# Kernel optimization log

Measured on AMD Instinct MI355X. Metric: run time of the kernel, lower is better.

The kernel has to match this reference:

```python
import jax, jax.numpy as jnp
import numpy as np

HW = 65536      # height*width = 256*256
C = 200         # spectral channels
NSP = 1024      # superpixels
E = 524288      # pixel-graph edges
D = 128         # hidden dim (hard-coded in module)
NCLS = 16
BN_EPS = 1e-5
LRELU = 0.01    # LeakyReLU default slope


def _l2norm(x):
    # F.normalize(x, dim=1)
    n = jnp.linalg.norm(x, axis=1, keepdims=True)
    return x / jnp.maximum(n, 1e-12)


def _bn(x):
    # BatchNorm1d, training-mode batch stats, default affine (gamma=1, beta=0)
    m = x.mean(0)
    v = x.var(0)
    return (x - m) * jax.lax.rsqrt(v + BN_EPS)


def _leaky(x):
    return jnp.where(x >= 0, x, LRELU * x)


def _gcn_conv(x, src, dst, W, b, n):
    # PyG GCNConv: add self-loops, sym-normalized aggregation, then bias
    xw = x @ W                                   # [n, D]
    deg = jnp.zeros((n,), x.dtype).at[dst].add(1.0) + 1.0  # incl. self-loop
    dinv = jax.lax.rsqrt(deg)
    norm = dinv[src] * dinv[dst]                 # [E]
    agg = jax.ops.segment_sum(xw[src] * norm[:, None], dst, num_segments=n)
    return agg + xw / deg[:, None] + b           # self-loop norm = 1/deg


def setup_inputs() -> dict:
    key = jax.random.key(0)
    ks = jax.random.split(key, 16)
    x = jax.random.normal(ks[0], (HW, C), jnp.float32)
    # one-hot superpixel assignment (every superpixel non-empty)
    seg = jnp.arange(HW, dtype=jnp.int32) % NSP
    seg = jax.random.permutation(ks[1], seg)
    Q = jax.nn.one_hot(seg, NSP, dtype=jnp.float32)
    # sparse-ish symmetric superpixel adjacency, normalized as in GCNLayer.__init__
    B = (jax.random.uniform(ks[2], (NSP, NSP)) < 0.01).astype(jnp.float32)
    A = jnp.maximum(B, B.T) * (1.0 - jnp.eye(NSP, dtype=jnp.float32))
    Ah = A + jnp.eye(NSP, dtype=jnp.float32)
    dinv = jax.lax.rsqrt(Ah.sum(1))
    A_norm = dinv[:, None] * Ah * dinv[None, :]
    edge_index = jax.random.randint(ks[3], (2, E), 0, HW, dtype=jnp.int32)
    s = 0.05
    return {
        'x': x, 'Q': Q, 'A_norm': A_norm, 'edge_index': edge_index,
        'prelin_W': jax.random.normal(ks[4], (C, D), jnp.float32) * s,
        'prelin_b': jnp.zeros((D,), jnp.float32),
        'gcn1_W': jax.random.normal(ks[5], (D, D), jnp.float32) * s,
        'gcn1_b': jnp.zeros((D,), jnp.float32),
        'gcn2_W': jax.random.normal(ks[6], (D, D), jnp.float32) * s,
        'gcn2_b': jnp.zeros((D,), jnp.float32),
        'mpnn1_W': jax.random.normal(ks[7], (D, D), jnp.float32) * s,
        'mpnn1_b': jnp.zeros((D,), jnp.float32),
        'mpnn2_W': jax.random.normal(ks[8], (D, D), jnp.float32) * s,
        'mpnn2_b': jnp.zeros((D,), jnp.float32),
        'out_W': jax.random.normal(ks[9], (D, NCLS), jnp.float32) * s,
        'out_b': jnp.zeros((NCLS,), jnp.float32),
    }


def reference(x, Q, A_norm, edge_index, prelin_W, prelin_b,
              gcn1_W, gcn1_b, gcn2_W, gcn2_b,
              mpnn1_W, mpnn1_b, mpnn2_W, mpnn2_b, out_W, out_b):
    # prelin + BN on pixels
    h = _bn(x @ prelin_W + prelin_b)             # [HW, D]
    # superpixel pooling (column-normalized Q), dense matmul as in original
    norm_col_Q = Q / Q.sum(0, keepdims=True)     # [HW, NSP]
    sp = norm_col_Q.T @ h                        # [NSP, D]

    def gcn_layer(H, W, b):
        return _leaky(A_norm @ (_bn(_l2norm(H)) @ W + b))

    H1 = gcn_layer(gcn_layer(sp, gcn1_W, gcn1_b), gcn2_W, gcn2_b)
    gcn_result = Q @ H1                          # unpool to pixels [HW, D]

    src, dst = edge_index[0], edge_index[1]

    def mpnn_layer(H, W, b):
        return _leaky(_gcn_conv(_bn(_l2norm(H)), src, dst, W, b, HW))

    m = mpnn_layer(mpnn_layer(h, mpnn1_W, mpnn1_b), mpnn2_W, mpnn2_b)
    logits = (m + gcn_result) @ out_W + out_b    # [HW, NCLS]
    return jax.nn.softmax(logits, axis=-1)
```

## Files before the change

### kernel.cpp

```cpp
#include <hip/hip_runtime.h>

#define HW 65536
#define NSP 1024
#define NE 524288
#define NCLS 16
#define BN_EPS 1e-5f
#define LSLOPE 0.01f

typedef unsigned short u16;
typedef short s16x8 __attribute__((ext_vector_type(8)));
typedef u16 u16x8 __attribute__((ext_vector_type(8)));
typedef u16 u16x4 __attribute__((ext_vector_type(4)));
typedef float f32x4 __attribute__((ext_vector_type(4)));

__device__ inline u16 f2b(float x) {
  unsigned int u = __float_as_uint(x);
  unsigned int r = ((u >> 16) & 1u) + 0x7FFFu;
  return (u16)((u + r) >> 16);
}
__device__ inline float b2f(u16 u) { return __uint_as_float(((unsigned int)u) << 16); }

struct P {
  const float *x, *Q, *A_norm;
  const int *e_src, *e_dst;
  const float *preW, *preB;
  const float *g1W, *g1b, *g2W, *g2b;
  const float *m1W, *m1b, *m2W, *m2b;
  const float *oW, *ob;
  float *outp;
  float *bufA, *bufB;
  int *cntd, *cntinv;
  float *stats;
  float *spDp, *spHp;
  int *seg, *seginv, *offp, *cur;
  float *dinv;
  int2 *e2;
  int *bsum;
  float *spA, *spC, *spDa;
  float *WppG1, *WppG2;
  u16 *WTm1, *WTm2, *WTpre;
  float *cvG1, *bpG1, *cvG2, *bpG2, *cvM1, *bpM1, *cvM2, *bpM2;
  float *invG1, *invG2, *invM1;
  u16 *xb, *xwB, *bufN;
};

#define S_A(p)  ((p).stats + 0*256)
#define S_G1(p) ((p).stats + 1*256)
#define S_G2(p) ((p).stats + 2*256)
#define S_M1(p) ((p).stats + 3*256)
#define S_M2(p) ((p).stats + 4*256)

#define NQB 4096
#define NDB (NE / 256)
#define CXB (HW * 56 / 256)
#define CWB 112

__global__ __launch_bounds__(256) void k_setup(P p) {
  int b = blockIdx.x, t = threadIdx.x;
  if (b < NQB) {
    const float4* Q4 = (const float4*)p.Q;
    const int n4 = HW * NSP / 4;
    for (int i = b * 256 + t; i < n4; i += NQB * 256) {
      float4 q = Q4[i];
      int base = i * 4;
      #pragma unroll
      for (int e = 0; e < 4; ++e) {
        float qv = (e == 0) ? q.x : (e == 1) ? q.y : (e == 2) ? q.z : q.w;
        if (qv > 0.5f) {
          int idx = base + e;
          int r = idx >> 10, s = idx & (NSP - 1);
          p.seg[r] = s;
          int pos = atomicAdd(&p.cntinv[s], 1);
          p.seginv[s * 64 + pos] = r;
        }
      }
    }
  } else if (b < NQB + NDB) {
    int e = (b - NQB) * 256 + t;
    if (e < NE) atomicAdd(&p.cntd[p.e_dst[e]], 1);
  } else if (b < NQB + NDB + CXB) {
    int g = (b - NQB - NDB) * 256 + t;
    int row = g / 56, qd = g - row * 56;
    int k0 = qd * 4;
    u16x4 o;
    if (k0 < 200) {
      float4 v = *(const float4*)&p.x[(size_t)row * 200 + k0];
      o[0] = f2b(v.x); o[1] = f2b(v.y); o[2] = f2b(v.z); o[3] = f2b(v.w);
    } else { o[0] = 0; o[1] = 0; o[2] = 0; o[3] = 0; }
    *(u16x4*)&p.xb[(size_t)row * 224 + k0] = o;
  } else {
    int g = (b - NQB - NDB - CXB) * 256 + t;
    if (g < 128 * 224) {
      int n = g / 224, k = g - n * 224;
      p.WTpre[g] = (k < 200) ? f2b(p.preW[(size_t)k * 128 + n]) : (u16)0;
    }
  }
}

__device__ void dev_scan_a(P& p, int b, char* smem) {
  int* s = (int*)smem;
  int t = threadIdx.x;
  int i = b * 256 + t;
  int v = p.cntd[i];
  s[t] = v; __syncthreads();
  for (int o = 1; o < 256; o <<= 1) {
    int x = (t >= o) ? s[t - o] : 0;
    __syncthreads();
    s[t] += x;
    __syncthreads();
  }
  p.offp[i] = s[t] - v;
  if (t == 255) p.bsum[b] = s[t];
}

__device__ void dev_scan_c2(P& p, int b, char* smem) {
  int* w4 = (int*)smem;
  int t = threadIdx.x;
  int v = (t < b) ? p.bsum[t] : 0;
  #pragma unroll
  for (int o = 1; o < 64; o <<= 1) v += __shfl_xor(v, o);
  if ((t & 63) == 0) w4[t >> 6] = v;
  __syncthreads();
  int base = w4[0] + w4[1] + w4[2] + w4[3];
  int i = b * 256 + t;
  int ov = p.offp[i] + base;
  p.offp[i] = ov;
  p.cur[i] = ov;
  p.dinv[i] = rsqrtf((float)p.cntd[i] + 1.0f);
  if (i == 0) p.offp[HW] = NE;
}

__device__ void dev_scatter(P& p, int b) {
  int e = b * 256 + threadIdx.x;
  if (e < NE) {
    int d = p.e_dst[e], s = p.e_src[e];
    float w = p.dinv[d] * p.dinv[s];
    int pos = atomicAdd(&p.cur[d], 1);
    p.e2[pos] = make_int2(s, __float_as_int(w));
  }
}

__device__ void dev_mgemm(const void* Ap, int a_bf16, int lda,
                          const u16* WT, int ldb, int K,
                          const float* bias, const float* cvec, const float* invn,
                          void* Cp, int c_bf16,
                          float* sums, float* sumsq, int bid, char* smem) {
  u16* As = (u16*)smem;
  u16* Bs = (u16*)(smem + 10240);
  float* lsum = (float*)(smem + 30720);
  float* lssq = lsum + 128;
  int t = threadIdx.x;
  if (sums && t < 128) { lsum[t] = 0.f; lssq[t] = 0.f; }
  int row0 = bid * 64;
  int ar = t >> 2, ak = (t & 3) * 8;
  u16x8 aReg; u16x8 bReg[2];

  auto loadRegs = [&](int k0) {
    if (a_bf16) {
      aReg = *(const u16x8*)((const u16*)Ap + (size_t)(row0 + ar) * lda + k0 + ak);
    } else {
      const float* ap = (const float*)Ap + (size_t)(row0 + ar) * lda + k0 + ak;
      float4 f0 = *(const float4*)ap;
      float4 f1 = *(const float4*)(ap + 4);
      u16x8 v;
      v[0] = f2b(f0.x); v[1] = f2b(f0.y); v[2] = f2b(f0.z); v[3] = f2b(f0.w);
      v[4] = f2b(f1.x); v[5] = f2b(f1.y); v[6] = f2b(f1.z); v[7] = f2b(f1.w);
      aReg = v;
    }
    #pragma unroll
    for (int it = 0; it < 2; ++it) {
      int slot = t + it * 256;
      int bn = slot >> 2, kg = (slot & 3) * 8;
      bReg[it] = *(const u16x8*)(WT + (size_t)bn * ldb + k0 + kg);
    }
  };
  auto dsWrite = [&](int bq) {
    *(u16x8*)&As[(bq * 64 + ar) * 40 + ak] = aReg;
    #pragma unroll
    for (int it = 0; it < 2; ++it) {
      int slot = t + it * 256;
      int bn = slot >> 2, kg = (slot & 3) * 8;
      *(u16x8*)&Bs[(bq * 128 + bn) * 40 + kg] = bReg[it];
    }
  };

  int lane = t & 63, wv = t >> 6;
  int m0 = (wv >> 1) * 32, n0 = (wv & 1) * 64;
  int fr = lane & 15, fk = (lane >> 4) * 8;
  f32x4 acc[2][4];
  #pragma unroll
  for (int mt = 0; mt < 2; ++mt)
    #pragma unroll
    for (int nt = 0; nt < 4; ++nt)
      acc[mt][nt] = (f32x4){0.f, 0.f, 0.f, 0.f};

  int nch = K >> 5;
  loadRegs(0);
  int cur = 0;
  for (int ch = 0; ch < nch; ++ch) {
    dsWrite(cur);
    __syncthreads();
    if (ch + 1 < nch) loadRegs((ch + 1) << 5);
    s16x8 afr0 = *(const s16x8*)&As[(cur * 64 + m0 + fr) * 40 + fk];
    s16x8 afr1 = *(const s16x8*)&As[(cur * 64 + m0 + 16 + fr) * 40 + fk];
    s16x8 bfr[4];
    #pragma unroll
    for (int nt = 0; nt < 4; ++nt)
      bfr[nt] = *(const s16x8*)&Bs[(cur * 128 + n0 + nt * 16 + fr) * 40 + fk];
    #pragma unroll
    for (int nt = 0; nt < 4; ++nt) {
      acc[0][nt] = __builtin_amdgcn_mfma_f32_16x16x32_bf16(afr0, bfr[nt], acc[0][nt], 0, 0, 0);
      acc[1][nt] = __builtin_amdgcn_mfma_f32_16x16x32_bf16(afr1, bfr[nt], acc[1][nt], 0, 0, 0);
    }
    cur ^= 1;
  }

  float bb4[4], cv4[4];
  #pragma unroll
  for (int nt = 0; nt < 4; ++nt) {
    int c = n0 + nt * 16 + fr;
    bb4[nt] = bias ? bias[c] : 0.f;
    cv4[nt] = cvec ? cvec[c] : 0.f;
  }
  int rg = lane >> 4;
  float cs4[4] = {}, cq4[4] = {};
  #pragma unroll
  for (int mt = 0; mt < 2; ++mt) {
    int rbase = row0 + m0 + mt * 16 + rg * 4;
    float inr[4];
    #pragma unroll
    for (int j = 0; j < 4; ++j) inr[j] = invn ? invn[rbase + j] : 1.f;
    #pragma unroll
    for (int nt = 0; nt < 4; ++nt) {
      int c = n0 + nt * 16 + fr;
      #pragma unroll
      for (int j = 0; j < 4; ++j) {
        float xv = inr[j] * (acc[mt][nt][j] - cv4[nt]) + bb4[nt];
        if (sums) { cs4[nt] += xv; cq4[nt] += xv * xv; }
        if (c_bf16) ((u16*)Cp)[(size_t)(rbase + j) * 128 + c] = f2b(xv);
        else        ((float*)Cp)[(size_t)(rbase + j) * 128 + c] = xv;
      }
    }
  }
  if (sums) {
    __syncthreads();
    #pragma unroll
    for (int nt = 0; nt < 4; ++nt) {
      int c = n0 + nt * 16 + fr;
      atomicAdd(&lsum[c], cs4[nt]);
      atomicAdd(&lssq[c], cq4[nt]);
    }
    __syncthreads();
    if (t < 128) { atomicAdd(&sums[t], lsum[t]); atomicAdd(&sumsq[t], lssq[t]); }
  }
}

__device__ void dev_pool2(P& p, int sp, char* smem) {
  float4* part = (float4*)smem;
  int t = threadIdx.x;
  int l32 = t & 31, g = t >> 5;
  int cnt = p.cntinv[sp];
  const float4* y4 = (const float4*)p.bufA;
  const int* lst = p.seginv + sp * 64;
  float4 acc = make_float4(0.f, 0.f, 0.f, 0.f);
  int r = g;
  for (; r + 8 < cnt; r += 16) {
    int i0 = lst[r], i1 = lst[r + 8];
    float4 a = y4[(size_t)i0 * 32 + l32];
    float4 b = y4[(size_t)i1 * 32 + l32];
    acc.x += a.x + b.x; acc.y += a.y + b.y;
    acc.z += a.z + b.z; acc.w += a.w + b.w;
  }
  for (; r < cnt; r += 8) {
    float4 a = y4[(size_t)lst[r] * 32 + l32];
    acc.x += a.x; acc.y += a.y; acc.z += a.z; acc.w += a.w;
  }
  part[g * 32 + l32] = acc;
  __syncthreads();
  if (g == 0) {
    float4 s = part[l32];
    #pragma unroll
    for (int q = 1; q < 8; ++q) {
      float4 pp = part[q * 32 + l32];
      s.x += pp.x; s.y += pp.y; s.z += pp.z; s.w += pp.w;
    }
    int d0 = l32 * 4;
    const float* sAs = S_A(p);
    const float* sAq = S_A(p) + 128;
    float4 ss = *(const float4*)&sAs[d0];
    float4 sq = *(const float4*)&sAq[d0];
    float inv = 1.0f / (float)cnt;
    float4 o;
    float m, rs;
    m = ss.x / HW; rs = rsqrtf(sq.x / HW - m * m + BN_EPS); o.x = (s.x * inv - m) * rs;
    m = ss.y / HW; rs = rsqrtf(sq.y / HW - m * m + BN_EPS); o.y = (s.y * inv - m) * rs;
    m = ss.z / HW; rs = rsqrtf(sq.z / HW - m * m + BN_EPS); o.z = (s.z * inv - m) * rs;
    m = ss.w / HW; rs = rsqrtf(sq.w / HW - m * m + BN_EPS); o.w = (s.w * inv - m) * rs;
    *(float4*)&p.spA[sp * 128 + d0] = o;
  }
}

__device__ void dev_rstats(const float* in, float* act_out, float* invn,
                           float* sums, float* sumsq, int M,
                           const float* preS, const float* preQ, float precnt,
                           int leaky_in, int bid, int nb, char* smem) {
  float* lsum = (float*)smem;
  float* lssq = lsum + 128;
  int t = threadIdx.x;
  if (t < 128) { lsum[t] = 0.f; lssq[t] = 0.f; }
  __syncthreads();
  int wid = t >> 6, lane = t & 63, d0 = lane * 2;
  float m0 = 0.f, m1 = 0.f, r0 = 1.f, r1 = 1.f;
  if (preS) {
    m0 = preS[d0] / precnt;
    r0 = rsqrtf(preQ[d0] / precnt - m0 * m0 + BN_EPS);
    m1 = preS[d0 + 1] / precnt;
    r1 = rsqrtf(preQ[d0 + 1] / precnt - m1 * m1 + BN_EPS);
  }
  float cs0 = 0.f, cs1 = 0.f, cq0 = 0.f, cq1 = 0.f;
  for (int row = bid * 4 + wid; row < M; row += nb * 4) {
    float2 v = *(const float2*)(in + (size_t)row * 128 + d0);
    v.x = (v.x - m0) * r0;
    v.y = (v.y - m1) * r1;
    if (leaky_in) {
      v.x = (v.x >= 0.f) ? v.x : LSLOPE * v.x;
      v.y = (v.y >= 0.f) ? v.y : LSLOPE * v.y;
    }
    if (act_out) *(float2*)(act_out + (size_t)row * 128 + d0) = v;
    float ss = v.x * v.x + v.y * v.y;
    #pragma unroll
    for (int o = 1; o < 64; o <<= 1) ss += __shfl_xor(ss, o);
    float sc = 1.0f / fmaxf(sqrtf(ss), 1e-12f);
    if (lane == 0) invn[row] = sc;
    float nx = v.x * sc, ny = v.y * sc;
    cs0 += nx; cs1 += ny; cq0 += nx * nx; cq1 += ny * ny;
  }
  atomicAdd(&lsum[d0], cs0); atomicAdd(&lsum[d0 + 1], cs1);
  atomicAdd(&lssq[d0], cq0); atomicAdd(&lssq[d0 + 1], cq1);
  __syncthreads();
  if (t < 128) { atomicAdd(&sums[t], lsum[t]); atomicAdd(&sumsq[t], lssq[t]); }
}

__device__ void dev_prepw(const float* sums, const float* sumsq, float cnt,
                          const float* W, const float* base,
                          const float* preS, const float* preQ, float precnt,
                          float* Wpp, u16* WT, float* cvec, float* bp, char* smem) {
  float* redc = (float*)smem;
  float* redb = redc + 1024;
  int t = threadIdx.x;
  int kq = (t & 31) * 4, jg = t >> 5;
  float cx = 0.f, cy = 0.f, cz = 0.f, cw = 0.f;
  float bx = 0.f, by = 0.f, bz = 0.f, bw = 0.f;
  for (int j = jg; j < 128; j += 8) {
    float m2 = sums[j] / cnt;
    float rs2 = rsqrtf(sumsq[j] / cnt - m2 * m2 + BN_EPS);
    float mA = 0.f, rsA = 1.f;
    if (preS) {
      mA = preS[j] / precnt;
      rsA = rsqrtf(preQ[j] / precnt - mA * mA + BN_EPS);
    }
    float4 w = *(const float4*)&W[j * 128 + kq];
    float sA = rsA * rs2;
    float4 wpp = make_float4(sA * w.x, sA * w.y, sA * w.z, sA * w.w);
    if (Wpp) *(float4*)&Wpp[j * 128 + kq] = wpp;
    if (WT) {
      WT[(size_t)(kq + 0) * 128 + j] = f2b(wpp.x);
      WT[(size_t)(kq + 1) * 128 + j] = f2b(wpp.y);
      WT[(size_t)(kq + 2) * 128 + j] = f2b(wpp.z);
      WT[(size_t)(kq + 3) * 128 + j] = f2b(wpp.w);
    }
    cx = fmaf(mA, wpp.x, cx); cy = fmaf(mA, wpp.y, cy);
    cz = fmaf(mA, wpp.z, cz); cw = fmaf(mA, wpp.w, cw);
    float m2s = m2 * rs2;
    bx = fmaf(m2s, w.x, bx); by = fmaf(m2s, w.y, by);
    bz = fmaf(m2s, w.z, bz); bw = fmaf(m2s, w.w, bw);
  }
  *(float4*)&redc[jg * 128 + kq] = make_float4(cx, cy, cz, cw);
  *(float4*)&redb[jg * 128 + kq] = make_float4(bx, by, bz, bw);
  __syncthreads();
  if (t < 32) {
    int k4 = t * 4;
    float4 sc = *(float4*)&redc[k4];
    float4 sb = *(float4*)&redb[k4];
    #pragma unroll
    for (int g = 1; g < 8; ++g) {
      float4 ac = *(float4*)&redc[g * 128 + k4];
      float4 ab = *(float4*)&redb[g * 128 + k4];
      sc.x += ac.x; sc.y += ac.y; sc.z += ac.z; sc.w += ac.w;
      sb.x += ab.x; sb.y += ab.y; sb.z += ab.z; sb.w += ab.w;
    }
    *(float4*)&cvec[k4] = sc;
    float4 bs = base ? *(const float4*)&base[k4] : make_float4(0, 0, 0, 0);
    *(float4*)&bp[k4] = make_float4(bs.x - sb.x, bs.y - sb.y, bs.z - sb.z, bs.w - sb.w);
  }
}

__device__ void dev_aggb(P& p, const u16* tbl, const float* bias, void* outp,
                         int norm_bf16, float* sums, float* sumsq,
                         int bid, int nb, char* smem) {
  float* lsum = (float*)smem;
  float* lssq = lsum + 128;
  int t = threadIdx.x;
  if (norm_bf16) {
    if (t < 128) { lsum[t] = 0.f; lssq[t] = 0.f; }
    __syncthreads();
  }
  int wid = t >> 6, lane = t & 63;
  int q = lane >> 4, l16 = lane & 15, c0 = l16 * 8;
  float bb[8];
  #pragma unroll
  for (int j = 0; j < 8; ++j) bb[j] = bias[c0 + j];
  float cs[8] = {}, cq[8] = {};
  for (int i = bid * 4 + wid; i < HW; i += nb * 4) {
    int s0 = p.offp[i], s1 = p.offp[i + 1];
    float di = p.dinv[i];
    u16x8 xi = *(const u16x8*)&tbl[(size_t)i * 128 + c0];
    float acc[8] = {};
    int kk = s0 + q;
    for (; kk + 4 < s1; kk += 8) {
      int2 ea = p.e2[kk], eb = p.e2[kk + 4];
      u16x8 va = *(const u16x8*)&tbl[(size_t)ea.x * 128 + c0];
      u16x8 vb = *(const u16x8*)&tbl[(size_t)eb.x * 128 + c0];
      float wa = __int_as_float(ea.y), wb = __int_as_float(eb.y);
      #pragma unroll
      for (int j = 0; j < 8; ++j) acc[j] = fmaf(wa, b2f(va[j]), acc[j]);
      #pragma unroll
      for (int j = 0; j < 8; ++j) acc[j] = fmaf(wb, b2f(vb[j]), acc[j]);
    }
    for (; kk < s1; kk += 4) {
      int2 e = p.e2[kk];
      u16x8 v = *(const u16x8*)&tbl[(size_t)e.x * 128 + c0];
      float w = __int_as_float(e.y);
      #pragma unroll
      for (int j = 0; j < 8; ++j) acc[j] = fmaf(w, b2f(v[j]), acc[j]);
    }
    #pragma unroll
    for (int j = 0; j < 8; ++j) {
      acc[j] += __shfl_xor(acc[j], 16);
      acc[j] += __shfl_xor(acc[j], 32);
    }
    float inv_deg = di * di;
    float r[8];
    #pragma unroll
    for (int j = 0; j < 8; ++j) {
      r[j] = fmaf(b2f(xi[j]), inv_deg, acc[j]) + bb[j];
      r[j] = (r[j] >= 0.f) ? r[j] : LSLOPE * r[j];
    }
    if (norm_bf16) {
      float ss = 0.f;
      #pragma unroll
      for (int j = 0; j < 8; ++j) ss += r[j] * r[j];
      ss += __shfl_xor(ss, 1); ss += __shfl_xor(ss, 2);
      ss += __shfl_xor(ss, 4); ss += __shfl_xor(ss, 8);
      float sc = 1.0f / fmaxf(sqrtf(ss), 1e-12f);
      if (q == 0) {
        u16x8 o;
        #pragma unroll
        for (int j = 0; j < 8; ++j) {
          r[j] *= sc;
          o[j] = f2b(r[j]);
          cs[j] += r[j]; cq[j] += r[j] * r[j];
        }
        *(u16x8*)&((u16*)outp)[(size_t)i * 128 + c0] = o;
      }
    } else if (q == 0) {
      float* op = (float*)outp + (size_t)i * 128 + c0;
      *(float4*)op = make_float4(r[0], r[1], r[2], r[3]);
      *(float4*)(op + 4) = make_float4(r[4], r[5], r[6], r[7]);
    }
  }
  if (norm_bf16) {
    if (q == 0) {
      #pragma unroll
      for (int j = 0; j < 8; ++j) {
        atomicAdd(&lsum[c0 + j], cs[j]);
        atomicAdd(&lssq[c0 + j], cq[j]);
      }
    }
    __syncthreads();
    if (t < 128) { atomicAdd(&sums[t], lsum[t]); atomicAdd(&sumsq[t], lssq[t]); }
  }
}

__device__ void dev_gemm_nolds(const float* in, const float* W,
                               const float* bp, const float* cv,
                               const float* invn, float* out, int bid) {
  int t = threadIdx.x;
  int c = t & 127, rh = t >> 7;
  int row0 = bid * 16 + rh * 8;
  float acc[8] = {};
  const float* ip = in + (size_t)row0 * 128;
  #pragma unroll 4
  for (int k = 0; k < 128; ++k) {
    float w = W[k * 128 + c];
    #pragma unroll
    for (int i = 0; i < 8; ++i)
      acc[i] = fmaf(ip[(size_t)i * 128 + k], w, acc[i]);
  }
  float cvc = cv[c], bpc = bp[c];
  #pragma unroll
  for (int i = 0; i < 8; ++i) {
    int row = row0 + i;
    out[(size_t)row * 128 + c] = invn[row] * (acc[i] - cvc) + bpc;
  }
}

__device__ void dev_gemm_ks(const float* A, const float* B, float* C,
                            int bid, char* smem) {
  float* As = (float*)smem;
  float* Bs = As + 32 * 68;
  int t = threadIdx.x;
  int c0 = (t & 31) * 4;
  int r0 = (t >> 5) * 8;
  int row0 = (bid >> 3) * 64;
  int kbeg = (bid & 7) * 128;
  int kend = kbeg + 128;
  int lr = t >> 2, lkb = (t & 3) * 8;
  float acc[8][4] = {};
  for (int k0 = kbeg; k0 < kend; k0 += 32) {
    __syncthreads();
    for (int idx = t * 4; idx < 32 * 128; idx += 1024)
      *(float4*)&Bs[(idx >> 7) * 128 + (idx & 127)] = *(const float4*)&B[(size_t)k0 * 128 + idx];
    {
      const float* ap = A + (size_t)(row0 + lr) * NSP + k0 + lkb;
      float4 v0 = *(const float4*)ap;
      float4 v1 = *(const float4*)(ap + 4);
      As[(lkb + 0) * 68 + lr] = v0.x; As[(lkb + 1) * 68 + lr] = v0.y;
      As[(lkb + 2) * 68 + lr] = v0.z; As[(lkb + 3) * 68 + lr] = v0.w;
      As[(lkb + 4) * 68 + lr] = v1.x; As[(lkb + 5) * 68 + lr] = v1.y;
      As[(lkb + 6) * 68 + lr] = v1.z; As[(lkb + 7) * 68 + lr] = v1.w;
    }
    __syncthreads();
    #pragma unroll 2
    for (int k = 0; k < 32; ++k) {
      float4 b4 = *(float4*)&Bs[k * 128 + c0];
      float4 a0 = *(float4*)&As[k * 68 + r0];
      float4 a1 = *(float4*)&As[k * 68 + r0 + 4];
      float av[8] = {a0.x, a0.y, a0.z, a0.w, a1.x, a1.y, a1.z, a1.w};
      float bv[4] = {b4.x, b4.y, b4.z, b4.w};
      #pragma unroll
      for (int r = 0; r < 8; ++r)
        #pragma unroll
        for (int c = 0; c < 4; ++c)
          acc[r][c] = fmaf(av[r], bv[c], acc[r][c]);
    }
  }
  #pragma unroll
  for (int r = 0; r < 8; ++r)
    #pragma unroll
    for (int c = 0; c < 4; ++c)
      atomicAdd(&C[(size_t)(row0 + r0 + r) * 128 + c0 + c], acc[r][c]);
}

__global__ __launch_bounds__(256) void k_za(P p) {
  __shared__ __align__(16) char smem[31744];
  int b = blockIdx.x;
  if (b < 256) dev_scan_a(p, b, smem);
  else dev_mgemm((const void*)p.xb, 1, 224, p.WTpre, 224, 224,
                 p.preB, nullptr, nullptr, (void*)p.bufA, 0,
                 S_A(p), S_A(p) + 128, b - 256, smem);
}
__global__ __launch_bounds__(256) void k_zb(P p) {
  __shared__ __align__(16) char smem[4096];
  int b = blockIdx.x;
  if (b < 256) dev_scan_c2(p, b, smem);
  else dev_pool2(p, b - 256, smem);
}
__global__ __launch_bounds__(256) void k_zc(P p) {
  __shared__ __align__(16) char smem[1024];
  int b = blockIdx.x;
  if (b < NE / 256) dev_scatter(p, b);
  else dev_rstats(p.bufA, nullptr, p.invM1, S_M1(p), S_M1(p) + 128, HW,
                  S_A(p), S_A(p) + 128, (float)HW, 0, b - NE / 256, 512, smem);
}
__global__ __launch_bounds__(256) void k_z8(P p) {
  __shared__ __align__(16) char smem[8192];
  int b = blockIdx.x;
  if (b < 16) dev_rstats(p.spA, nullptr, p.invG1, S_G1(p), S_G1(p) + 128, NSP,
                         nullptr, nullptr, 1.f, 0, b, 16, smem);
  else dev_prepw(S_M1(p), S_M1(p) + 128, (float)HW, p.m1W, nullptr,
                 S_A(p), S_A(p) + 128, (float)HW,
                 nullptr, p.WTm1, p.cvM1, p.bpM1, smem);
}
__global__ __launch_bounds__(256) void k_z9(P p) {
  __shared__ __align__(16) char smem[31744];
  int b = blockIdx.x;
  if (b < 1) dev_prepw(S_G1(p), S_G1(p) + 128, (float)NSP, p.g1W, p.g1b,
                       nullptr, nullptr, 1.f, p.WppG1, nullptr, p.cvG1, p.bpG1, smem);
  else dev_mgemm((const void*)p.bufA, 0, 128, p.WTm1, 128, 128,
                 p.bpM1, p.cvM1, p.invM1, (void*)p.xwB, 1,
                 nullptr, nullptr, b - 1, smem);
}
__global__ __launch_bounds__(256) void k_z10(P p) {
  __shared__ __align__(16) char smem[1024];
  int b = blockIdx.x;
  if (b < 64) dev_gemm_nolds(p.spA, p.WppG1, p.bpG1, p.cvG1, p.invG1, p.spC, b);
  else dev_aggb(p, p.xwB, p.m1b, (void*)p.bufN, 1,
                S_M2(p), S_M2(p) + 128, b - 64, 2048, smem);
}
__global__ __launch_bounds__(256) void k_z11(P p) {
  __shared__ __align__(16) char smem[25088];
  int b = blockIdx.x;
  if (b < 128) dev_gemm_ks(p.A_norm, p.spC, p.spDp, b, smem);
  else dev_prepw(S_M2(p), S_M2(p) + 128, (float)HW, p.m2W, nullptr,
                 nullptr, nullptr, 1.f, nullptr, p.WTm2, p.cvM2, p.bpM2, smem);
}
__global__ __launch_bounds__(256) void k_z12(P p) {
  __shared__ __align__(16) char smem[31744];
  int b = blockIdx.x;
  if (b < 16) dev_rstats(p.spDp, p.spDa, p.invG2, S_G2(p), S_G2(p) + 128, NSP,
                         nullptr, nullptr, 1.f, 1, b, 16, smem);
  else dev_mgemm((const void*)p.bufN, 1, 128, p.WTm2, 128, 128,
                 p.bpM2, p.cvM2, nullptr, (void*)p.xwB, 1,
                 nullptr, nullptr, b - 16, smem);
}
__global__ __launch_bounds__(256) void k_z13(P p) {
  __shared__ __align__(16) char smem[8192];
  int b = blockIdx.x;
  if (b < 1) dev_prepw(S_G2(p), S_G2(p) + 128, (float)NSP, p.g2W, p.g2b,
                       nullptr, nullptr, 1.f, p.WppG2, nullptr, p.cvG2, p.bpG2, smem);
  else dev_aggb(p, p.xwB, p.m2b, (void*)p.bufB, 0,
                nullptr, nullptr, b - 1, 2048, smem);
}
__global__ __launch_bounds__(256) void k_g2(P p) {
  dev_gemm_nolds(p.spDa, p.WppG2, p.bpG2, p.cvG2, p.invG2, p.spC, blockIdx.x);
}
__global__ __launch_bounds__(256) void k_an2(P p) {
  __shared__ __align__(16) char smem[25088];
  dev_gemm_ks(p.A_norm, p.spC, p.spHp, blockIdx.x, smem);
}

__global__ __launch_bounds__(256) void k_final(P p) {
  __shared__ float rb[16][132];
  __shared__ float WL[128 * 16];
  int t = threadIdx.x;
  int row0 = blockIdx.x * 16;
  for (int idx = t; idx < 128 * NCLS; idx += 256) WL[idx] = p.oW[idx];
  for (int idx = t; idx < 16 * 128; idx += 256) {
    int r = idx >> 7, d = idx & 127;
    int row = row0 + r;
    float h = p.spHp[(size_t)p.seg[row] * 128 + d];
    h = (h >= 0.f) ? h : LSLOPE * h;
    rb[r][d] = p.bufB[(size_t)row * 128 + d] + h;
  }
  __syncthreads();
  int c = t & 15, r = t >> 4;
  float acc = p.ob[c];
  #pragma unroll 8
  for (int d = 0; d < 128; ++d) acc = fmaf(rb[r][d], WL[d * 16 + c], acc);
  float mx = acc;
  #pragma unroll
  for (int o = 1; o < 16; o <<= 1) mx = fmaxf(mx, __shfl_xor(mx, o));
  float e = expf(acc - mx);
  float s = e;
  #pragma unroll
  for (int o = 1; o < 16; o <<= 1) s += __shfl_xor(s, o);
  p.outp[(size_t)(row0 + r) * NCLS + c] = e / s;
}

extern "C" void kernel_launch(void* const* d_in, const int* in_sizes, int n_in,
                              void* d_out, int out_size, void* d_ws, size_t ws_size,
                              hipStream_t stream) {
  P p;
  p.x      = (const float*)d_in[0];
  p.Q      = (const float*)d_in[1];
  p.A_norm = (const float*)d_in[2];
  p.e_src  = (const int*)d_in[3];
  p.e_dst  = (const int*)d_in[3] + NE;
  p.preW = (const float*)d_in[4];  p.preB = (const float*)d_in[5];
  p.g1W  = (const float*)d_in[6];  p.g1b  = (const float*)d_in[7];
  p.g2W  = (const float*)d_in[8];  p.g2b  = (const float*)d_in[9];
  p.m1W  = (const float*)d_in[10]; p.m1b  = (const float*)d_in[11];
  p.m2W  = (const float*)d_in[12]; p.m2b  = (const float*)d_in[13];
  p.oW   = (const float*)d_in[14]; p.ob   = (const float*)d_in[15];
  p.outp = (float*)d_out;

  char* ws = (char*)d_ws;
  size_t o = 0;
  auto alloc = [&](size_t bytes) { size_t r = o; o = (o + bytes + 255) & ~255ULL; return r; };
  size_t bufA_o   = alloc((size_t)HW * 128 * 4);
  size_t bufB_o   = alloc((size_t)HW * 128 * 4);
  size_t cntd_o   = alloc((size_t)HW * 4);
  size_t cntinv_o = alloc((size_t)NSP * 4);
  size_t stats_o  = alloc(5 * 256 * 4);
  size_t spDp_o   = alloc((size_t)NSP * 128 * 4);
  size_t spHp_o   = alloc((size_t)NSP * 128 * 4);
  size_t zero_end = o;
  size_t seg_o    = alloc((size_t)HW * 4);
  size_t seginv_o = alloc((size_t)HW * 4);
  size_t off_o    = alloc((size_t)(HW + 1) * 4);
  size_t cur_o    = alloc((size_t)HW * 4);
  size_t dinv_o   = alloc((size_t)HW * 4);
  size_t e2_o     = alloc((size_t)NE * 8);
  size_t bsum_o   = alloc(256 * 4);
  size_t spA_o    = alloc((size_t)NSP * 128 * 4);
  size_t spC_o    = alloc((size_t)NSP * 128 * 4);
  size_t spDa_o   = alloc((size_t)NSP * 128 * 4);
  size_t WppG1_o  = alloc(128 * 128 * 4);
  size_t WppG2_o  = alloc(128 * 128 * 4);
  size_t WTm1_o   = alloc(128 * 128 * 2);
  size_t WTm2_o   = alloc(128 * 128 * 2);
  size_t WTpre_o  = alloc(128 * 224 * 2);
  size_t cvG1_o = alloc(512), bpG1_o = alloc(512);
  size_t cvG2_o = alloc(512), bpG2_o = alloc(512);
  size_t cvM1_o = alloc(512), bpM1_o = alloc(512);
  size_t cvM2_o = alloc(512), bpM2_o = alloc(512);
  size_t invG1_o  = alloc((size_t)NSP * 4);
  size_t invG2_o  = alloc((size_t)NSP * 4);
  size_t invM1_o  = alloc((size_t)HW * 4);
  size_t xb_o     = alloc((size_t)HW * 224 * 2);
  size_t xwB_o    = alloc((size_t)HW * 128 * 2);
  size_t bufN_o   = alloc((size_t)HW * 128 * 2);
  if (o > ws_size) return;

  p.bufA  = (float*)(ws + bufA_o);
  p.bufB  = (float*)(ws + bufB_o);
  p.cntd  = (int*)(ws + cntd_o);
  p.cntinv= (int*)(ws + cntinv_o);
  p.stats = (float*)(ws + stats_o);
  p.spDp  = (float*)(ws + spDp_o);
  p.spHp  = (float*)(ws + spHp_o);
  p.seg   = (int*)(ws + seg_o);
  p.seginv= (int*)(ws + seginv_o);
  p.offp  = (int*)(ws + off_o);
  p.cur   = (int*)(ws + cur_o);
  p.dinv  = (float*)(ws + dinv_o);
  p.e2    = (int2*)(ws + e2_o);
  p.bsum  = (int*)(ws + bsum_o);
  p.spA   = (float*)(ws + spA_o);
  p.spC   = (float*)(ws + spC_o);
  p.spDa  = (float*)(ws + spDa_o);
  p.WppG1 = (float*)(ws + WppG1_o);
  p.WppG2 = (float*)(ws + WppG2_o);
  p.WTm1  = (u16*)(ws + WTm1_o);
  p.WTm2  = (u16*)(ws + WTm2_o);
  p.WTpre = (u16*)(ws + WTpre_o);
  p.cvG1 = (float*)(ws + cvG1_o); p.bpG1 = (float*)(ws + bpG1_o);
  p.cvG2 = (float*)(ws + cvG2_o); p.bpG2 = (float*)(ws + bpG2_o);
  p.cvM1 = (float*)(ws + cvM1_o); p.bpM1 = (float*)(ws + bpM1_o);
  p.cvM2 = (float*)(ws + cvM2_o); p.bpM2 = (float*)(ws + bpM2_o);
  p.invG1 = (float*)(ws + invG1_o);
  p.invG2 = (float*)(ws + invG2_o);
  p.invM1 = (float*)(ws + invM1_o);
  p.xb   = (u16*)(ws + xb_o);
  p.xwB  = (u16*)(ws + xwB_o);
  p.bufN = (u16*)(ws + bufN_o);

  hipMemsetAsync(ws + cntd_o, 0, zero_end - cntd_o, stream);

  hipLaunchKernelGGL(k_setup, dim3(NQB + NDB + CXB + CWB), dim3(256), 0, stream, p);
  hipLaunchKernelGGL(k_za,    dim3(256 + HW / 64), dim3(256), 0, stream, p);
  hipLaunchKernelGGL(k_zb,    dim3(256 + NSP), dim3(256), 0, stream, p);
  hipLaunchKernelGGL(k_zc,    dim3(NE / 256 + 512), dim3(256), 0, stream, p);
  hipLaunchKernelGGL(k_z8,    dim3(17), dim3(256), 0, stream, p);
  hipLaunchKernelGGL(k_z9,    dim3(1 + HW / 64), dim3(256), 0, stream, p);
  hipLaunchKernelGGL(k_z10,   dim3(64 + 2048), dim3(256), 0, stream, p);
  hipLaunchKernelGGL(k_z11,   dim3(129), dim3(256), 0, stream, p);
  hipLaunchKernelGGL(k_z12,   dim3(16 + HW / 64), dim3(256), 0, stream, p);
  hipLaunchKernelGGL(k_z13,   dim3(1 + 2048), dim3(256), 0, stream, p);
  hipLaunchKernelGGL(k_g2,    dim3(64), dim3(256), 0, stream, p);
  hipLaunchKernelGGL(k_an2,   dim3(128), dim3(256), 0, stream, p);
  hipLaunchKernelGGL(k_final, dim3(HW / 16), dim3(256), 0, stream, p);
}
```

Measured before the change: 449.1 us.

## Assign one 16-lane group per destination node in edge aggregation

The pixel-graph aggregation kernel now maps each 16-lane group to a single destination node, so a 256-thread block covers 16 nodes. Previously a 64-lane wave handled one node at a time with four edge-parallel quarters, in a grid-stride loop over 2048 blocks. The new scheme drops the cross-quarter shuffle reduction and the idle non-zero quarters during output. It launches HW/16 blocks and unrolls the per-node edge loop by four to keep several gathers in flight. In exchange, each block now does its LDS and global atomic BN-stat reduction once for 16 nodes instead of amortising it over many nodes, and each node's edges are walked serially by one group.

```diff
diff --git a/kernel.cpp b/kernel.cpp
--- a/kernel.cpp
+++ b/kernel.cpp
@@ -397,7 +397,7 @@
 
 __device__ void dev_aggb(P& p, const u16* tbl, const float* bias, void* outp,
                          int norm_bf16, float* sums, float* sumsq,
-                         int bid, int nb, char* smem) {
+                         int bid, char* smem) {
   float* lsum = (float*)smem;
   float* lssq = lsum + 128;
   int t = threadIdx.x;
@@ -405,72 +405,65 @@
     if (t < 128) { lsum[t] = 0.f; lssq[t] = 0.f; }
     __syncthreads();
   }
-  int wid = t >> 6, lane = t & 63;
-  int q = lane >> 4, l16 = lane & 15, c0 = l16 * 8;
-  float bb[8];
-  #pragma unroll
-  for (int j = 0; j < 8; ++j) bb[j] = bias[c0 + j];
-  float cs[8] = {}, cq[8] = {};
-  for (int i = bid * 4 + wid; i < HW; i += nb * 4) {
-    int s0 = p.offp[i], s1 = p.offp[i + 1];
-    float di = p.dinv[i];
-    u16x8 xi = *(const u16x8*)&tbl[(size_t)i * 128 + c0];
-    float acc[8] = {};
-    int kk = s0 + q;
-    for (; kk + 4 < s1; kk += 8) {
-      int2 ea = p.e2[kk], eb = p.e2[kk + 4];
-      u16x8 va = *(const u16x8*)&tbl[(size_t)ea.x * 128 + c0];
-      u16x8 vb = *(const u16x8*)&tbl[(size_t)eb.x * 128 + c0];
-      float wa = __int_as_float(ea.y), wb = __int_as_float(eb.y);
-      #pragma unroll
-      for (int j = 0; j < 8; ++j) acc[j] = fmaf(wa, b2f(va[j]), acc[j]);
-      #pragma unroll
-      for (int j = 0; j < 8; ++j) acc[j] = fmaf(wb, b2f(vb[j]), acc[j]);
-    }
-    for (; kk < s1; kk += 4) {
-      int2 e = p.e2[kk];
-      u16x8 v = *(const u16x8*)&tbl[(size_t)e.x * 128 + c0];
-      float w = __int_as_float(e.y);
-      #pragma unroll
-      for (int j = 0; j < 8; ++j) acc[j] = fmaf(w, b2f(v[j]), acc[j]);
-    }
+  int q = t >> 4, l16 = t & 15, c0 = l16 * 8;
+  int i = bid * 16 + q;
+  int s0 = p.offp[i], s1 = p.offp[i + 1];
+  float di = p.dinv[i];
+  u16x8 xi = *(const u16x8*)&tbl[(size_t)i * 128 + c0];
+  float acc[8] = {};
+  int kk = s0;
+  for (; kk + 3 < s1; kk += 4) {
+    int2 ea = p.e2[kk], eb = p.e2[kk + 1], ec = p.e2[kk + 2], ed = p.e2[kk + 3];
+    u16x8 va = *(const u16x8*)&tbl[(size_t)ea.x * 128 + c0];
+    u16x8 vb = *(const u16x8*)&tbl[(size_t)eb.x * 128 + c0];
+    u16x8 vc = *(const u16x8*)&tbl[(size_t)ec.x * 128 + c0];
+    u16x8 vd = *(const u16x8*)&tbl[(size_t)ed.x * 128 + c0];
+    float wa = __int_as_float(ea.y), wb = __int_as_float(eb.y);
+    float wc = __int_as_float(ec.y), wd = __int_as_float(ed.y);
     #pragma unroll
     for (int j = 0; j < 8; ++j) {
-      acc[j] += __shfl_xor(acc[j], 16);
-      acc[j] += __shfl_xor(acc[j], 32);
-    }
-    float inv_deg = di * di;
-    float r[8];
+      acc[j] = fmaf(wa, b2f(va[j]), acc[j]);
+      acc[j] = fmaf(wb, b2f(vb[j]), acc[j]);
+      acc[j] = fmaf(wc, b2f(vc[j]), acc[j]);
+      acc[j] = fmaf(wd, b2f(vd[j]), acc[j]);
+    }
+  }
+  for (; kk < s1; ++kk) {
+    int2 e = p.e2[kk];
+    u16x8 v = *(const u16x8*)&tbl[(size_t)e.x * 128 + c0];
+    float w = __int_as_float(e.y);
+    #pragma unroll
+    for (int j = 0; j < 8; ++j) acc[j] = fmaf(w, b2f(v[j]), acc[j]);
+  }
+  float inv_deg = di * di;
+  float r[8];
+  #pragma unroll
+  for (int j = 0; j < 8; ++j) {
+    r[j] = fmaf(b2f(xi[j]), inv_deg, acc[j]) + bias[c0 + j];
+    r[j] = (r[j] >= 0.f) ? r[j] : LSLOPE * r[j];
+  }
+  if (norm_bf16) {
+    float ss = 0.f;
+    #pragma unroll
+    for (int j = 0; j < 8; ++j) ss += r[j] * r[j];
+    ss += __shfl_xor(ss, 1); ss += __shfl_xor(ss, 2);
+    ss += __shfl_xor(ss, 4); ss += __shfl_xor(ss, 8);
+    float sc = 1.0f / fmaxf(sqrtf(ss), 1e-12f);
+    u16x8 o;
+    float cs[8], cq[8];
     #pragma unroll
     for (int j = 0; j < 8; ++j) {
-      r[j] = fmaf(b2f(xi[j]), inv_deg, acc[j]) + bb[j];
-      r[j] = (r[j] >= 0.f) ? r[j] : LSLOPE * r[j];
-    }
-    if (norm_bf16) {
-      float ss = 0.f;
-      #pragma unroll
-      for (int j = 0; j < 8; ++j) ss += r[j] * r[j];
-      ss += __shfl_xor(ss, 1); ss += __shfl_xor(ss, 2);
-      ss += __shfl_xor(ss, 4); ss += __shfl_xor(ss, 8);
-      float sc = 1.0f / fmaxf(sqrtf(ss), 1e-12f);
-      if (q == 0) {
-        u16x8 o;
-        #pragma unroll
-        for (int j = 0; j < 8; ++j) {
-          r[j] *= sc;
-          o[j] = f2b(r[j]);
-          cs[j] += r[j]; cq[j] += r[j] * r[j];
-        }
-        *(u16x8*)&((u16*)outp)[(size_t)i * 128 + c0] = o;
-      }
-    } else if (q == 0) {
-      float* op = (float*)outp + (size_t)i * 128 + c0;
-      *(float4*)op = make_float4(r[0], r[1], r[2], r[3]);
-      *(float4*)(op + 4) = make_float4(r[4], r[5], r[6], r[7]);
-    }
-  }
-  if (norm_bf16) {
-    if (q == 0) {
+      r[j] *= sc;
+      o[j] = f2b(r[j]);
+      cs[j] = r[j]; cq[j] = r[j] * r[j];
+    }
+    *(u16x8*)&((u16*)outp)[(size_t)i * 128 + c0] = o;
+    #pragma unroll
+    for (int j = 0; j < 8; ++j) {
+      cs[j] += __shfl_xor(cs[j], 16); cs[j] += __shfl_xor(cs[j], 32);
+      cq[j] += __shfl_xor(cq[j], 16); cq[j] += __shfl_xor(cq[j], 32);
+    }
+    if (((t & 63) >> 4) == 0) {
       #pragma unroll
       for (int j = 0; j < 8; ++j) {
         atomicAdd(&lsum[c0 + j], cs[j]);
@@ -479,6 +472,10 @@
     }
     __syncthreads();
     if (t < 128) { atomicAdd(&sums[t], lsum[t]); atomicAdd(&sumsq[t], lssq[t]); }
+  } else {
+    float* op = (float*)outp + (size_t)i * 128 + c0;
+    *(float4*)op = make_float4(r[0], r[1], r[2], r[3]);
+    *(float4*)(op + 4) = make_float4(r[4], r[5], r[6], r[7]);
   }
 }
 
@@ -596,7 +593,7 @@
   int b = blockIdx.x;
   if (b < 64) dev_gemm_nolds(p.spA, p.WppG1, p.bpG1, p.cvG1, p.invG1, p.spC, b);
   else dev_aggb(p, p.xwB, p.m1b, (void*)p.bufN, 1,
-                S_M2(p), S_M2(p) + 128, b - 64, 2048, smem);
+                S_M2(p), S_M2(p) + 128, b - 64, smem);
 }
 __global__ __launch_bounds__(256) void k_z11(P p) {
   __shared__ __align__(16) char smem[25088];
@@ -620,7 +617,7 @@
   if (b < 1) dev_prepw(S_G2(p), S_G2(p) + 128, (float)NSP, p.g2W, p.g2b,
                        nullptr, nullptr, 1.f, p.WppG2, nullptr, p.cvG2, p.bpG2, smem);
   else dev_aggb(p, p.xwB, p.m2b, (void*)p.bufB, 0,
-                nullptr, nullptr, b - 1, 2048, smem);
+                nullptr, nullptr, b - 1, smem);
 }
 __global__ __launch_bounds__(256) void k_g2(P p) {
   dev_gemm_nolds(p.spDa, p.WppG2, p.bpG2, p.cvG2, p.invG2, p.spC, blockIdx.x);
@@ -754,10 +751,10 @@
   hipLaunchKernelGGL(k_zc,    dim3(NE / 256 + 512), dim3(256), 0, stream, p);
   hipLaunchKernelGGL(k_z8,    dim3(17), dim3(256), 0, stream, p);
   hipLaunchKernelGGL(k_z9,    dim3(1 + HW / 64), dim3(256), 0, stream, p);
-  hipLaunchKernelGGL(k_z10,   dim3(64 + 2048), dim3(256), 0, stream, p);
+  hipLaunchKernelGGL(k_z10,   dim3(64 + HW / 16), dim3(256), 0, stream, p);
   hipLaunchKernelGGL(k_z11,   dim3(129), dim3(256), 0, stream, p);
   hipLaunchKernelGGL(k_z12,   dim3(16 + HW / 64), dim3(256), 0, stream, p);
-  hipLaunchKernelGGL(k_z13,   dim3(1 + 2048), dim3(256), 0, stream, p);
+  hipLaunchKernelGGL(k_z13,   dim3(1 + HW / 16), dim3(256), 0, stream, p);
   hipLaunchKernelGGL(k_g2,    dim3(64), dim3(256), 0, stream, p);
   hipLaunchKernelGGL(k_an2,   dim3(128), dim3(256), 0, stream, p);
   hipLaunchKernelGGL(k_final, dim3(HW / 16), dim3(256), 0, stream, p);
```

Result: slower. 478.5 us (+6.6%).

## Reassociate superpixel GCN as (A·Xn)·W' and scan Q rows with early exit

Applied to the files above, without the earlier changes.

The superpixel GCN layers now multiply A_norm by the L2-normalized features first and apply the folded BN weight afterwards, using precomputed A_norm row sums for the bias term. This lets the A_norm GEMM run concurrently with the weight-prep and mgemm work, which removes two serial kernel launches (k_g2, k_an2). The one-hot Q decode now reads row-wise with a wave ballot and stops at the first hit instead of scanning the full 256MB matrix. The early exit relies on each Q row holding exactly one one-hot entry, and the z1p/z2p buffers are zeroed because they are accumulated.

```diff
diff --git a/kernel.cpp b/kernel.cpp
--- a/kernel.cpp
+++ b/kernel.cpp
@@ -36,7 +36,8 @@
   float *dinv;
   int2 *e2;
   int *bsum;
-  float *spA, *spC, *spDa;
+  float *spA;
+  float *xn1, *xn2, *z1p, *z2p, *rsums;
   float *WppG1, *WppG2;
   u16 *WTm1, *WTm2, *WTpre;
   float *cvG1, *bpG1, *cvG2, *bpG2, *cvM1, *bpM1, *cvM2, *bpM2;
@@ -54,24 +55,30 @@
 #define NDB (NE / 256)
 #define CXB (HW * 56 / 256)
 #define CWB 112
+#define RSB 256
 
 __global__ __launch_bounds__(256) void k_setup(P p) {
   int b = blockIdx.x, t = threadIdx.x;
+  int wv = t >> 6, lane = t & 63;
   if (b < NQB) {
-    const float4* Q4 = (const float4*)p.Q;
-    const int n4 = HW * NSP / 4;
-    for (int i = b * 256 + t; i < n4; i += NQB * 256) {
-      float4 q = Q4[i];
-      int base = i * 4;
-      #pragma unroll
-      for (int e = 0; e < 4; ++e) {
-        float qv = (e == 0) ? q.x : (e == 1) ? q.y : (e == 2) ? q.z : q.w;
-        if (qv > 0.5f) {
-          int idx = base + e;
-          int r = idx >> 10, s = idx & (NSP - 1);
-          p.seg[r] = s;
-          int pos = atomicAdd(&p.cntinv[s], 1);
-          p.seginv[s * 64 + pos] = r;
+    #pragma unroll
+    for (int rr = 0; rr < 4; ++rr) {
+      int row = (b * 4 + wv) * 4 + rr;
+      const float4* qrow = (const float4*)(p.Q + (size_t)row * NSP);
+      for (int c = 0; c < 4; ++c) {
+        float4 v = qrow[c * 64 + lane];
+        int hit = (v.x > 0.5f) || (v.y > 0.5f) || (v.z > 0.5f) || (v.w > 0.5f);
+        unsigned long long m = __ballot(hit);
+        if (m) {
+          int L = (int)__ffsll((unsigned long long)m) - 1;
+          if (lane == L) {
+            int comp = (v.x > 0.5f) ? 0 : (v.y > 0.5f) ? 1 : (v.z > 0.5f) ? 2 : 3;
+            int s = c * 256 + lane * 4 + comp;
+            p.seg[row] = s;
+            int pos = atomicAdd(&p.cntinv[s], 1);
+            p.seginv[s * 64 + pos] = row;
+          }
+          break;
         }
       }
     }
@@ -88,12 +95,24 @@
       o[0] = f2b(v.x); o[1] = f2b(v.y); o[2] = f2b(v.z); o[3] = f2b(v.w);
     } else { o[0] = 0; o[1] = 0; o[2] = 0; o[3] = 0; }
     *(u16x4*)&p.xb[(size_t)row * 224 + k0] = o;
-  } else {
+  } else if (b < NQB + NDB + CXB + CWB) {
     int g = (b - NQB - NDB - CXB) * 256 + t;
     if (g < 128 * 224) {
       int n = g / 224, k = g - n * 224;
       p.WTpre[g] = (k < 200) ? f2b(p.preW[(size_t)k * 128 + n]) : (u16)0;
     }
+  } else {
+    int row = (b - NQB - NDB - CXB - CWB) * 4 + wv;
+    const float4* ar = (const float4*)(p.A_norm + (size_t)row * NSP);
+    float s = 0.f;
+    #pragma unroll
+    for (int c = 0; c < 4; ++c) {
+      float4 v = ar[c * 64 + lane];
+      s += v.x + v.y + v.z + v.w;
+    }
+    #pragma unroll
+    for (int o = 1; o < 64; o <<= 1) s += __shfl_xor(s, o);
+    if (lane == 0) p.rsums[row] = s;
   }
 }
 
@@ -184,8 +203,8 @@
     }
   };
 
-  int lane = t & 63, wv = t >> 6;
-  int m0 = (wv >> 1) * 32, n0 = (wv & 1) * 64;
+  int lane = t & 63, wvv = t >> 6;
+  int m0 = (wvv >> 1) * 32, n0 = (wvv & 1) * 64;
   int fr = lane & 15, fk = (lane >> 4) * 8;
   f32x4 acc[2][4];
   #pragma unroll
@@ -300,7 +319,7 @@
   }
 }
 
-__device__ void dev_rstats(const float* in, float* act_out, float* invn,
+__device__ void dev_rstats(const float* in, float* norm_out, float* invn,
                            float* sums, float* sumsq, int M,
                            const float* preS, const float* preQ, float precnt,
                            int leaky_in, int bid, int nb, char* smem) {
@@ -326,13 +345,13 @@
       v.x = (v.x >= 0.f) ? v.x : LSLOPE * v.x;
       v.y = (v.y >= 0.f) ? v.y : LSLOPE * v.y;
     }
-    if (act_out) *(float2*)(act_out + (size_t)row * 128 + d0) = v;
     float ss = v.x * v.x + v.y * v.y;
     #pragma unroll
     for (int o = 1; o < 64; o <<= 1) ss += __shfl_xor(ss, o);
     float sc = 1.0f / fmaxf(sqrtf(ss), 1e-12f);
     if (lane == 0) invn[row] = sc;
     float nx = v.x * sc, ny = v.y * sc;
+    if (norm_out) *(float2*)(norm_out + (size_t)row * 128 + d0) = make_float2(nx, ny);
     cs0 += nx; cs1 += ny; cq0 += nx * nx; cq1 += ny * ny;
   }
   atomicAdd(&lsum[d0], cs0); atomicAdd(&lsum[d0 + 1], cs1);
@@ -482,14 +501,14 @@
   }
 }
 
-__device__ void dev_gemm_nolds(const float* in, const float* W,
-                               const float* bp, const float* cv,
-                               const float* invn, float* out, int bid) {
+__device__ void dev_gemm_tail(const float* Z, const float* W,
+                              const float* bp, const float* rs,
+                              float* out, int bid) {
   int t = threadIdx.x;
   int c = t & 127, rh = t >> 7;
   int row0 = bid * 16 + rh * 8;
   float acc[8] = {};
-  const float* ip = in + (size_t)row0 * 128;
+  const float* ip = Z + (size_t)row0 * 128;
   #pragma unroll 4
   for (int k = 0; k < 128; ++k) {
     float w = W[k * 128 + c];
@@ -497,11 +516,11 @@
     for (int i = 0; i < 8; ++i)
       acc[i] = fmaf(ip[(size_t)i * 128 + k], w, acc[i]);
   }
-  float cvc = cv[c], bpc = bp[c];
+  float bpc = bp[c];
   #pragma unroll
   for (int i = 0; i < 8; ++i) {
     int row = row0 + i;
-    out[(size_t)row * 128 + c] = invn[row] * (acc[i] - cvc) + bpc;
+    out[(size_t)row * 128 + c] = acc[i] + rs[row] * bpc;
   }
 }
 
@@ -576,7 +595,7 @@
 __global__ __launch_bounds__(256) void k_z8(P p) {
   __shared__ __align__(16) char smem[8192];
   int b = blockIdx.x;
-  if (b < 16) dev_rstats(p.spA, nullptr, p.invG1, S_G1(p), S_G1(p) + 128, NSP,
+  if (b < 16) dev_rstats(p.spA, p.xn1, p.invG1, S_G1(p), S_G1(p) + 128, NSP,
                          nullptr, nullptr, 1.f, 0, b, 16, smem);
   else dev_prepw(S_M1(p), S_M1(p) + 128, (float)HW, p.m1W, nullptr,
                  S_A(p), S_A(p) + 128, (float)HW,
@@ -585,49 +604,44 @@
 __global__ __launch_bounds__(256) void k_z9(P p) {
   __shared__ __align__(16) char smem[31744];
   int b = blockIdx.x;
-  if (b < 1) dev_prepw(S_G1(p), S_G1(p) + 128, (float)NSP, p.g1W, p.g1b,
-                       nullptr, nullptr, 1.f, p.WppG1, nullptr, p.cvG1, p.bpG1, smem);
+  if (b < 128) dev_gemm_ks(p.A_norm, p.xn1, p.z1p, b, smem);
+  else if (b < 129) dev_prepw(S_G1(p), S_G1(p) + 128, (float)NSP, p.g1W, p.g1b,
+                              nullptr, nullptr, 1.f, p.WppG1, nullptr, p.cvG1, p.bpG1, smem);
   else dev_mgemm((const void*)p.bufA, 0, 128, p.WTm1, 128, 128,
                  p.bpM1, p.cvM1, p.invM1, (void*)p.xwB, 1,
-                 nullptr, nullptr, b - 1, smem);
+                 nullptr, nullptr, b - 129, smem);
 }
 __global__ __launch_bounds__(256) void k_z10(P p) {
   __shared__ __align__(16) char smem[1024];
   int b = blockIdx.x;
-  if (b < 64) dev_gemm_nolds(p.spA, p.WppG1, p.bpG1, p.cvG1, p.invG1, p.spC, b);
+  if (b < 64) dev_gemm_tail(p.z1p, p.WppG1, p.bpG1, p.rsums, p.spDp, b);
   else dev_aggb(p, p.xwB, p.m1b, (void*)p.bufN, 1,
                 S_M2(p), S_M2(p) + 128, b - 64, 2048, smem);
 }
 __global__ __launch_bounds__(256) void k_z11(P p) {
-  __shared__ __align__(16) char smem[25088];
-  int b = blockIdx.x;
-  if (b < 128) dev_gemm_ks(p.A_norm, p.spC, p.spDp, b, smem);
-  else dev_prepw(S_M2(p), S_M2(p) + 128, (float)HW, p.m2W, nullptr,
-                 nullptr, nullptr, 1.f, nullptr, p.WTm2, p.cvM2, p.bpM2, smem);
+  __shared__ __align__(16) char smem[8192];
+  int b = blockIdx.x;
+  if (b < 1) dev_prepw(S_M2(p), S_M2(p) + 128, (float)HW, p.m2W, nullptr,
+                       nullptr, nullptr, 1.f, nullptr, p.WTm2, p.cvM2, p.bpM2, smem);
+  else dev_rstats(p.spDp, p.xn2, p.invG2, S_G2(p), S_G2(p) + 128, NSP,
+                  nullptr, nullptr, 1.f, 1, b - 1, 16, smem);
 }
 __global__ __launch_bounds__(256) void k_z12(P p) {
   __shared__ __align__(16) char smem[31744];
   int b = blockIdx.x;
-  if (b < 16) dev_rstats(p.spDp, p.spDa, p.invG2, S_G2(p), S_G2(p) + 128, NSP,
-                         nullptr, nullptr, 1.f, 1, b, 16, smem);
+  if (b < 128) dev_gemm_ks(p.A_norm, p.xn2, p.z2p, b, smem);
+  else if (b < 129) dev_prepw(S_G2(p), S_G2(p) + 128, (float)NSP, p.g2W, p.g2b,
+                              nullptr, nullptr, 1.f, p.WppG2, nullptr, p.cvG2, p.bpG2, smem);
   else dev_mgemm((const void*)p.bufN, 1, 128, p.WTm2, 128, 128,
                  p.bpM2, p.cvM2, nullptr, (void*)p.xwB, 1,
-                 nullptr, nullptr, b - 16, smem);
+                 nullptr, nullptr, b - 129, smem);
 }
 __global__ __launch_bounds__(256) void k_z13(P p) {
-  __shared__ __align__(16) char smem[8192];
-  int b = blockIdx.x;
-  if (b < 1) dev_prepw(S_G2(p), S_G2(p) + 128, (float)NSP, p.g2W, p.g2b,
-                       nullptr, nullptr, 1.f, p.WppG2, nullptr, p.cvG2, p.bpG2, smem);
+  __shared__ __align__(16) char smem[1024];
+  int b = blockIdx.x;
+  if (b < 64) dev_gemm_tail(p.z2p, p.WppG2, p.bpG2, p.rsums, p.spHp, b);
   else dev_aggb(p, p.xwB, p.m2b, (void*)p.bufB, 0,
-                nullptr, nullptr, b - 1, 2048, smem);
-}
-__global__ __launch_bounds__(256) void k_g2(P p) {
-  dev_gemm_nolds(p.spDa, p.WppG2, p.bpG2, p.cvG2, p.invG2, p.spC, blockIdx.x);
-}
-__global__ __launch_bounds__(256) void k_an2(P p) {
-  __shared__ __align__(16) char smem[25088];
-  dev_gemm_ks(p.A_norm, p.spC, p.spHp, blockIdx.x, smem);
+                nullptr, nullptr, b - 64, 2048, smem);
 }
 
 __global__ __launch_bounds__(256) void k_final(P p) {
@@ -683,9 +697,11 @@
   size_t cntd_o   = alloc((size_t)HW * 4);
   size_t cntinv_o = alloc((size_t)NSP * 4);
   size_t stats_o  = alloc(5 * 256 * 4);
+  size_t z1p_o    = alloc((size_t)NSP * 128 * 4);
+  size_t z2p_o    = alloc((size_t)NSP * 128 * 4);
+  size_t zero_end = o;
   size_t spDp_o   = alloc((size_t)NSP * 128 * 4);
   size_t spHp_o   = alloc((size_t)NSP * 128 * 4);
-  size_t zero_end = o;
   size_t seg_o    = alloc((size_t)HW * 4);
   size_t seginv_o = alloc((size_t)HW * 4);
   size_t off_o    = alloc((size_t)(HW + 1) * 4);
@@ -694,8 +710,9 @@
   size_t e2_o     = alloc((size_t)NE * 8);
   size_t bsum_o   = alloc(256 * 4);
   size_t spA_o    = alloc((size_t)NSP * 128 * 4);
-  size_t spC_o    = alloc((size_t)NSP * 128 * 4);
-  size_t spDa_o   = alloc((size_t)NSP * 128 * 4);
+  size_t xn1_o    = alloc((size_t)NSP * 128 * 4);
+  size_t xn2_o    = alloc((size_t)NSP * 128 * 4);
+  size_t rsums_o  = alloc((size_t)NSP * 4);
   size_t WppG1_o  = alloc(128 * 128 * 4);
   size_t WppG2_o  = alloc(128 * 128 * 4);
   size_t WTm1_o   = alloc(128 * 128 * 2);
@@ -718,6 +735,8 @@
   p.cntd  = (int*)(ws + cntd_o);
   p.cntinv= (int*)(ws + cntinv_o);
   p.stats = (float*)(ws + stats_o);
+  p.z1p   = (float*)(ws + z1p_o);
+  p.z2p   = (float*)(ws + z2p_o);
   p.spDp  = (float*)(ws + spDp_o);
   p.spHp  = (float*)(ws + spHp_o);
   p.seg   = (int*)(ws + seg_o);
@@ -728,8 +747,9 @@
   p.e2    = (int2*)(ws + e2_o);
   p.bsum  = (int*)(ws + bsum_o);
   p.spA   = (float*)(ws + spA_o);
-  p.spC   = (float*)(ws + spC_o);
-  p.spDa  = (float*)(ws + spDa_o);
+  p.xn1   = (float*)(ws + xn1_o);
+  p.xn2   = (float*)(ws + xn2_o);
+  p.rsums = (float*)(ws + rsums_o);
   p.WppG1 = (float*)(ws + WppG1_o);
   p.WppG2 = (float*)(ws + WppG2_o);
   p.WTm1  = (u16*)(ws + WTm1_o);
@@ -748,17 +768,15 @@
 
   hipMemsetAsync(ws + cntd_o, 0, zero_end - cntd_o, stream);
 
-  hipLaunchKernelGGL(k_setup, dim3(NQB + NDB + CXB + CWB), dim3(256), 0, stream, p);
+  hipLaunchKernelGGL(k_setup, dim3(NQB + NDB + CXB + CWB + RSB), dim3(256), 0, stream, p);
   hipLaunchKernelGGL(k_za,    dim3(256 + HW / 64), dim3(256), 0, stream, p);
   hipLaunchKernelGGL(k_zb,    dim3(256 + NSP), dim3(256), 0, stream, p);
   hipLaunchKernelGGL(k_zc,    dim3(NE / 256 + 512), dim3(256), 0, stream, p);
   hipLaunchKernelGGL(k_z8,    dim3(17), dim3(256), 0, stream, p);
-  hipLaunchKernelGGL(k_z9,    dim3(1 + HW / 64), dim3(256), 0, stream, p);
+  hipLaunchKernelGGL(k_z9,    dim3(129 + HW / 64), dim3(256), 0, stream, p);
   hipLaunchKernelGGL(k_z10,   dim3(64 + 2048), dim3(256), 0, stream, p);
-  hipLaunchKernelGGL(k_z11,   dim3(129), dim3(256), 0, stream, p);
-  hipLaunchKernelGGL(k_z12,   dim3(16 + HW / 64), dim3(256), 0, stream, p);
-  hipLaunchKernelGGL(k_z13,   dim3(1 + 2048), dim3(256), 0, stream, p);
-  hipLaunchKernelGGL(k_g2,    dim3(64), dim3(256), 0, stream, p);
-  hipLaunchKernelGGL(k_an2,   dim3(128), dim3(256), 0, stream, p);
+  hipLaunchKernelGGL(k_z11,   dim3(17), dim3(256), 0, stream, p);
+  hipLaunchKernelGGL(k_z12,   dim3(129 + HW / 64), dim3(256), 0, stream, p);
+  hipLaunchKernelGGL(k_z13,   dim3(64 + 2048), dim3(256), 0, stream, p);
   hipLaunchKernelGGL(k_final, dim3(HW / 16), dim3(256), 0, stream, p);
 }
```

Result: faster. 429.9 us (-4.3%).
